# Kernel tuning notes

Measured on AMD Instinct MI355X. Metric: run time of the kernel, lower is better.

Reference implementation:

```python
import jax, jax.numpy as jnp
import numpy as np

B, T, C = 2, 2048, 1024
N_HEAD, N_GROUP = 16, 4
N_KV = N_HEAD // N_GROUP          # 4
HEAD_DIM = C // N_HEAD            # 64
ROPE_BASE = 10000.0
INIT_STD = 0.02


def setup_inputs() -> dict:
    key = jax.random.key(0)
    ks = jax.random.split(key, 5)
    kvC = N_KV * HEAD_DIM
    return {
        "x": jax.random.normal(ks[0], (B, T, C), jnp.float32),
        "w_q": jax.random.normal(ks[1], (C, C), jnp.float32) * INIT_STD,
        "b_q": jnp.zeros((C,), jnp.float32),
        "w_k": jax.random.normal(ks[2], (C, kvC), jnp.float32) * INIT_STD,
        "b_k": jnp.zeros((kvC,), jnp.float32),
        "w_v": jax.random.normal(ks[3], (C, kvC), jnp.float32) * INIT_STD,
        "b_v": jnp.zeros((kvC,), jnp.float32),
        "w_o": jax.random.normal(ks[4], (C, C), jnp.float32) * INIT_STD,
        "b_o": jnp.zeros((C,), jnp.float32),
    }


def reference(x, w_q, b_q, w_k, b_k, w_v, b_v, w_o, b_o):
    Bx, Tx, Cx = x.shape
    # projections (torch Linear math with weights stored as [in, out])
    q = (x @ w_q + b_q).reshape(Bx, Tx, N_HEAD, HEAD_DIM).transpose(0, 2, 1, 3)  # [B,H,T,hd]
    k = (x @ w_k + b_k).reshape(Bx, Tx, N_KV, HEAD_DIM).transpose(0, 2, 1, 3)    # [B,KV,T,hd]
    v = (x @ w_v + b_v).reshape(Bx, Tx, N_KV, HEAD_DIM).transpose(0, 2, 1, 3)

    # RoPE with INTERLEAVED pair convention: pairs are (dim 2i, dim 2i+1)
    inv_freq = 1.0 / (ROPE_BASE ** (jnp.arange(0, HEAD_DIM, 2, dtype=jnp.float32) / HEAD_DIM))
    freqs = jnp.arange(Tx, dtype=jnp.float32)[:, None] * inv_freq[None, :]       # [T, hd/2]
    cos, sin = jnp.cos(freqs), jnp.sin(freqs)

    def rope(t):
        tp = t.reshape(*t.shape[:-1], HEAD_DIM // 2, 2)
        e, o = tp[..., 0], tp[..., 1]          # even/odd lanes, [B,h,T,hd/2]
        er = e * cos - o * sin
        orr = e * sin + o * cos
        return jnp.stack([er, orr], axis=-1).reshape(t.shape)

    q, k = rope(q), rope(k)

    # GQA: duplicate each KV head n_group times (consecutively, like repeat_interleave)
    k = jnp.repeat(k, N_GROUP, axis=1)   # [B,H,T,hd]
    v = jnp.repeat(v, N_GROUP, axis=1)

    attn = jnp.einsum('bhqd,bhkd->bhqk', q, k) / np.sqrt(HEAD_DIM).astype(np.float32)
    causal = jnp.tril(jnp.ones((Tx, Tx), bool))
    attn = jnp.where(causal, attn, -jnp.inf)
    attn = jax.nn.softmax(attn, axis=-1)

    out = jnp.einsum('bhqk,bhkd->bhqd', attn, v)            # [B,H,T,hd]
    out = out.transpose(0, 2, 1, 3).reshape(Bx, Tx, Cx)
    return out @ w_o + b_o
```

## Files before the change

kernel.cpp:

```cpp
#include <hip/hip_runtime.h>
#include <hip/hip_bf16.h>

typedef __hip_bfloat16 bf16;
typedef __attribute__((ext_vector_type(8))) short short8_t;
typedef __attribute__((ext_vector_type(4))) short short4_t;
typedef __attribute__((ext_vector_type(4))) float f32x4;

#define B_SZ   2
#define T_SEQ  2048
#define C_DIM  1024
#define NH     16
#define NKV    4
#define HD     64
#define QKVW   1536

#define LOG2_BASE_OVER_32 0.4152410118609203f
#define Q_SCALE 0.1803368801111204f

__device__ __forceinline__ short f2bs(float f) {
    unsigned u = __float_as_uint(f);
    u += 0x7FFFu + ((u >> 16) & 1u);
    return (short)(u >> 16);
}
__device__ __forceinline__ short f2bs_trunc(float f) {
    return (short)(__float_as_uint(f) >> 16);
}
__device__ __forceinline__ float bs2f(short s) {
    unsigned u = ((unsigned)(unsigned short)s) << 16;
    return __uint_as_float(u);
}

__device__ __forceinline__ void store_c(float* p, float v) { *p = v; }
__device__ __forceinline__ void store_c(short* p, float v) { *p = f2bs(v); }

__device__ __forceinline__ void transpose_tile(
    const float* __restrict__ W, short* __restrict__ Wt,
    int K, int N, int n0, int k0, int tid)
{
    __shared__ float tile[32][33];
    int tx = tid & 31, ty = tid >> 5;
    #pragma unroll
    for (int i = 0; i < 4; ++i)
        tile[ty + 8 * i][tx] = W[(size_t)(k0 + ty + 8 * i) * N + n0 + tx];
    __syncthreads();
    #pragma unroll
    for (int i = 0; i < 4; ++i)
        Wt[(size_t)(n0 + ty + 8 * i) * K + k0 + tx] = f2bs(tile[tx][ty + 8 * i]);
}

__global__ __launch_bounds__(256) void prep_kernel(
    const float* __restrict__ x,
    const float* __restrict__ w_q, const float* __restrict__ w_k,
    const float* __restrict__ w_v, const float* __restrict__ w_o,
    const float* __restrict__ b_q, const float* __restrict__ b_k,
    const float* __restrict__ b_v,
    short* __restrict__ Xb, short* __restrict__ Wqkv, short* __restrict__ Wto,
    float* __restrict__ Bqkv, float2* __restrict__ Tab)
{
    int blk = blockIdx.x, tid = threadIdx.x;
    if (blk < 4096) {
        int i = blk * 1024 + tid * 4;
        float4 v = *(const float4*)(x + i);
        short4_t o;
        o[0] = f2bs(v.x); o[1] = f2bs(v.y); o[2] = f2bs(v.z); o[3] = f2bs(v.w);
        *(short4_t*)(Xb + i) = o;
    } else if (blk < 5120) {
        int l = blk - 4096;
        transpose_tile(w_q, Wqkv, C_DIM, C_DIM, (l & 31) * 32, (l >> 5) * 32, tid);
    } else if (blk < 5376) {
        int l = blk - 5120;
        transpose_tile(w_k, Wqkv + (size_t)1024 * C_DIM, C_DIM, 256,
                       (l & 7) * 32, (l >> 3) * 32, tid);
    } else if (blk < 5632) {
        int l = blk - 5376;
        transpose_tile(w_v, Wqkv + (size_t)1280 * C_DIM, C_DIM, 256,
                       (l & 7) * 32, (l >> 3) * 32, tid);
    } else if (blk < 6656) {
        int l = blk - 5632;
        transpose_tile(w_o, Wto, C_DIM, C_DIM, (l & 31) * 32, (l >> 5) * 32, tid);
    } else if (blk < 6662) {
        int i = (blk - 6656) * 256 + tid;
        float v;
        if (i < 1024)      v = b_q[i];
        else if (i < 1280) v = b_k[i - 1024];
        else               v = b_v[i - 1280];
        Bqkv[i] = v;
    } else {
        int idx = (blk - 6662) * 256 + tid;
        int t = idx >> 5, i = idx & 31;
        float ang = (float)t * exp2f(-(float)i * LOG2_BASE_OVER_32);
        Tab[idx] = make_float2(cosf(ang), sinf(ang));
    }
}

template <typename CT>
__global__ __launch_bounds__(256) void gemm_mfma_bt(
    const short* __restrict__ A, const short* __restrict__ Bt,
    const float* __restrict__ bias, CT* __restrict__ C,
    int M, int N, int K)
{
    __shared__ __align__(16) short sA[2][128][40];
    __shared__ __align__(16) short sB[2][128][40];

    int m0 = blockIdx.y * 128;
    int n0 = blockIdx.x * 128;
    int tid  = threadIdx.x;
    int w    = tid >> 6, lane = tid & 63;
    int quad = lane >> 4, l16 = lane & 15;
    int wm = w & 1, wn = w >> 1;

    f32x4 acc[4][4] = {};

    short8_t ra[2], rb[2];
    #pragma unroll
    for (int it = 0; it < 2; ++it) {
        int slot = tid + 256 * it, row = slot >> 2, g = (slot & 3) * 8;
        ra[it] = *(const short8_t*)(A  + (size_t)(m0 + row) * K + g);
        rb[it] = *(const short8_t*)(Bt + (size_t)(n0 + row) * K + g);
    }

    int buf = 0;
    for (int k0 = 0; k0 < K; k0 += 32, buf ^= 1) {
        #pragma unroll
        for (int it = 0; it < 2; ++it) {
            int slot = tid + 256 * it, row = slot >> 2, g = (slot & 3) * 8;
            *(short8_t*)&sA[buf][row][g] = ra[it];
            *(short8_t*)&sB[buf][row][g] = rb[it];
        }
        if (k0 + 32 < K) {
            #pragma unroll
            for (int it = 0; it < 2; ++it) {
                int slot = tid + 256 * it, row = slot >> 2, g = (slot & 3) * 8;
                ra[it] = *(const short8_t*)(A  + (size_t)(m0 + row) * K + k0 + 32 + g);
                rb[it] = *(const short8_t*)(Bt + (size_t)(n0 + row) * K + k0 + 32 + g);
            }
        }
        __syncthreads();

        short8_t af[4], bfr[4];
        #pragma unroll
        for (int mt = 0; mt < 4; ++mt)
            af[mt] = *(const short8_t*)&sA[buf][wm * 64 + mt * 16 + l16][quad * 8];
        #pragma unroll
        for (int nt = 0; nt < 4; ++nt)
            bfr[nt] = *(const short8_t*)&sB[buf][wn * 64 + nt * 16 + l16][quad * 8];
        #pragma unroll
        for (int mt = 0; mt < 4; ++mt)
            #pragma unroll
            for (int nt = 0; nt < 4; ++nt)
                acc[mt][nt] = __builtin_amdgcn_mfma_f32_16x16x32_bf16(
                    af[mt], bfr[nt], acc[mt][nt], 0, 0, 0);
    }

    #pragma unroll
    for (int mt = 0; mt < 4; ++mt) {
        #pragma unroll
        for (int nt = 0; nt < 4; ++nt) {
            int col = n0 + wn * 64 + nt * 16 + l16;
            float bv = bias[col];
            #pragma unroll
            for (int r = 0; r < 4; ++r) {
                int row = m0 + wm * 64 + mt * 16 + quad * 4 + r;
                store_c(&C[(size_t)row * N + col], acc[mt][nt][r] + bv);
            }
        }
    }
}

__global__ __launch_bounds__(256) void rope_k_transpose_v(
    short* __restrict__ QKV, const float2* __restrict__ Tab,
    short* __restrict__ Vt)
{
    int blk = blockIdx.x, tid = threadIdx.x;
    if (blk < 2048) {
        int g = blk * 256 + tid;
        int row = g >> 7, pi = g & 127;
        int col = 1024 + pi * 2;
        int t = row & (T_SEQ - 1);
        int i = pi & 31;
        size_t base = (size_t)row * QKVW + col;
        float e = bs2f(QKV[base]);
        float o = bs2f(QKV[base + 1]);
        float2 cs = Tab[t * 32 + i];
        QKV[base]     = f2bs(e * cs.x - o * cs.y);
        QKV[base + 1] = f2bs(e * cs.y + o * cs.x);
    } else {
        __shared__ __align__(16) short sT[64][72];
        int l = blk - 2048;
        int d0 = (l >> 6) * 64;
        int r0 = (l & 63) * 64;
        int i0 = tid >> 3, seg = (tid & 7) * 8;
        #pragma unroll
        for (int it = 0; it < 2; ++it) {
            int i = i0 + 32 * it;
            *(short8_t*)&sT[i][seg] =
                *(const short8_t*)(QKV + (size_t)(r0 + i) * QKVW + 1280 + d0 + seg);
        }
        __syncthreads();
        #pragma unroll
        for (int it = 0; it < 2; ++it) {
            int d = i0 + 32 * it;
            short8_t o;
            #pragma unroll
            for (int k = 0; k < 8; ++k) o[k] = sT[seg + k][d];
            *(short8_t*)(Vt + (size_t)(d0 + d) * (B_SZ * T_SEQ) + r0 + seg) = o;
        }
    }
}

__global__ __launch_bounds__(256) void attn_mfma6(
    const short* __restrict__ QKV, const short* __restrict__ Vt,
    const float2* __restrict__ Tab, short* __restrict__ O)
{
    __shared__ __align__(16) short sK [64][72];
    __shared__ __align__(16) short sVt[64][72];
    __shared__ __align__(16) short sP [4][16][72];

    const int tid  = threadIdx.x;
    const int w    = tid >> 6;
    const int lane = tid & 63;
    const int quad = lane >> 4;
    const int l16  = lane & 15;

    int blk = blockIdx.x;
    int grp = blk & 7;
    int tq  = 127 - (blk >> 3);
    int kvh = grp & 3;
    int b   = grp >> 2;
    int h   = kvh * 4 + w;
    int ct  = tq >> 2;

    const short* qptr = QKV + ((size_t)(b * T_SEQ + tq * 16 + l16)) * QKVW + h * HD;
    short8_t q0r = *(const short8_t*)(qptr + quad * 8);
    short8_t q1r = *(const short8_t*)(qptr + quad * 8 + 32);
    int tg = tq * 16 + l16;
    const float2* tb = Tab + tg * 32 + quad * 4;
    short8_t qf0, qf1;
    #pragma unroll
    for (int j = 0; j < 4; ++j) {
        float2 cs0 = tb[j];
        float e0 = bs2f(q0r[2 * j]), o0 = bs2f(q0r[2 * j + 1]);
        qf0[2 * j]     = f2bs((e0 * cs0.x - o0 * cs0.y) * Q_SCALE);
        qf0[2 * j + 1] = f2bs((e0 * cs0.y + o0 * cs0.x) * Q_SCALE);
        float2 cs1 = tb[j + 16];
        float e1 = bs2f(q1r[2 * j]), o1 = bs2f(q1r[2 * j + 1]);
        qf1[2 * j]     = f2bs((e1 * cs1.x - o1 * cs1.y) * Q_SCALE);
        qf1[2 * j + 1] = f2bs((e1 * cs1.y + o1 * cs1.x) * Q_SCALE);
    }

    const short* kbase  = QKV + (size_t)b * T_SEQ * QKVW + 1024 + kvh * HD;
    const short* vtbase = Vt + (size_t)(kvh * HD) * (B_SZ * T_SEQ) + b * T_SEQ;

    float m_l = -INFINITY, l_l = 0.f;
    f32x4 oacc[4];
    #pragma unroll
    for (int dt = 0; dt < 4; ++dt) oacc[dt] = (f32x4){0.f, 0.f, 0.f, 0.f};

    const int kkey = tid >> 3, kd = (tid & 7) * 8;
    const int vdim = tid >> 3, vseg = (tid & 7) * 8;

    short8_t kr[2], vr[2];
    #pragma unroll
    for (int it = 0; it < 2; ++it) {
        kr[it] = *(const short8_t*)(kbase + (size_t)(kkey + 32 * it) * QKVW + kd);
        vr[it] = *(const short8_t*)(vtbase + (size_t)(vdim + 32 * it) * (B_SZ * T_SEQ) + vseg);
    }

    for (int c = 0; c <= ct; ++c) {
        __syncthreads();
        #pragma unroll
        for (int it = 0; it < 2; ++it) {
            *(short8_t*)&sK [kkey + 32 * it][kd]   = kr[it];
            *(short8_t*)&sVt[vdim + 32 * it][vseg] = vr[it];
        }
        __syncthreads();
        if (c < ct) {
            int jn = (c + 1) * 64;
            #pragma unroll
            for (int it = 0; it < 2; ++it) {
                kr[it] = *(const short8_t*)(kbase + (size_t)(jn + kkey + 32 * it) * QKVW + kd);
                vr[it] = *(const short8_t*)(vtbase + (size_t)(vdim + 32 * it) * (B_SZ * T_SEQ) + jn + vseg);
            }
        }

        f32x4 sacc[4];
        #pragma unroll
        for (int kt = 0; kt < 4; ++kt) {
            f32x4 z = {0.f, 0.f, 0.f, 0.f};
            short8_t kf0 = *(const short8_t*)&sK[l16 + 16 * kt][quad * 8];
            short8_t kf1 = *(const short8_t*)&sK[l16 + 16 * kt][quad * 8 + 32];
            z = __builtin_amdgcn_mfma_f32_16x16x32_bf16(kf0, qf0, z, 0, 0, 0);
            z = __builtin_amdgcn_mfma_f32_16x16x32_bf16(kf1, qf1, z, 0, 0, 0);
            sacc[kt] = z;
        }

        if (c == ct) {
            int j0 = c * 64;
            #pragma unroll
            for (int kt = 0; kt < 4; ++kt)
                #pragma unroll
                for (int r = 0; r < 4; ++r)
                    if (j0 + 16 * kt + quad * 4 + r > tg) sacc[kt][r] = -INFINITY;
        }

        float vmax = sacc[0][0];
        #pragma unroll
        for (int kt = 0; kt < 4; ++kt)
            #pragma unroll
            for (int r = 0; r < 4; ++r) vmax = fmaxf(vmax, sacc[kt][r]);
        vmax = fmaxf(vmax, __shfl_xor(vmax, 16));
        vmax = fmaxf(vmax, __shfl_xor(vmax, 32));
        float mnew = fmaxf(m_l, vmax);
        float al = exp2f(m_l - mnew);
        m_l = mnew;

        float psum = 0.f;
        #pragma unroll
        for (int kt = 0; kt < 4; ++kt) {
            short4_t pk;
            #pragma unroll
            for (int r = 0; r < 4; ++r) {
                float p = exp2f(sacc[kt][r] - mnew);
                psum += p;
                pk[r] = f2bs_trunc(p);
            }
            *(short4_t*)&sP[w][l16][16 * kt + 4 * quad] = pk;
        }
        psum += __shfl_xor(psum, 16);
        psum += __shfl_xor(psum, 32);
        l_l = l_l * al + psum;

        if (__any(al < 1.f)) {
            #pragma unroll
            for (int r = 0; r < 4; ++r) {
                float alr = __shfl(al, quad * 4 + r);
                #pragma unroll
                for (int dt = 0; dt < 4; ++dt) oacc[dt][r] *= alr;
            }
        }

        short8_t pf0 = *(const short8_t*)&sP[w][l16][quad * 8];
        short8_t pf1 = *(const short8_t*)&sP[w][l16][quad * 8 + 32];
        #pragma unroll
        for (int dt = 0; dt < 4; ++dt) {
            short8_t vf0 = *(const short8_t*)&sVt[16 * dt + l16][quad * 8];
            short8_t vf1 = *(const short8_t*)&sVt[16 * dt + l16][quad * 8 + 32];
            oacc[dt] = __builtin_amdgcn_mfma_f32_16x16x32_bf16(pf0, vf0, oacc[dt], 0, 0, 0);
            oacc[dt] = __builtin_amdgcn_mfma_f32_16x16x32_bf16(pf1, vf1, oacc[dt], 0, 0, 0);
        }
    }

    #pragma unroll
    for (int r = 0; r < 4; ++r) {
        int m = quad * 4 + r;
        float lr = __shfl(l_l, quad * 4 + r);
        float inv = __builtin_amdgcn_rcpf(lr);
        #pragma unroll
        for (int dt = 0; dt < 4; ++dt)
            O[((size_t)b * T_SEQ + tq * 16 + m) * C_DIM + h * HD + 16 * dt + l16] =
                f2bs(oacc[dt][r] * inv);
    }
}

extern "C" void kernel_launch(void* const* d_in, const int* in_sizes, int n_in,
                              void* d_out, int out_size, void* d_ws, size_t ws_size,
                              hipStream_t stream)
{
    const float* x   = (const float*)d_in[0];
    const float* w_q = (const float*)d_in[1];
    const float* b_q = (const float*)d_in[2];
    const float* w_k = (const float*)d_in[3];
    const float* b_k = (const float*)d_in[4];
    const float* w_v = (const float*)d_in[5];
    const float* b_v = (const float*)d_in[6];
    const float* w_o = (const float*)d_in[7];
    const float* b_o = (const float*)d_in[8];
    float* out = (float*)d_out;

    char* ws = (char*)d_ws;
    short*  Xb   = (short*) (ws);
    short*  Ab   = (short*) (ws + ((size_t)8  << 20));
    short*  QKVb = (short*) (ws + ((size_t)16 << 20));
    short*  Wqkv = (short*) (ws + ((size_t)28 << 20));
    short*  Wto  = (short*) (ws + ((size_t)31 << 20));
    float*  Bqkv = (float*) (ws + ((size_t)33 << 20));
    float2* Tab  = (float2*)(ws + ((size_t)33 << 20) + 8192);
    short*  Vt   = (short*) (ws + ((size_t)34 << 20));

    const int M = B_SZ * T_SEQ;

    prep_kernel<<<6918, 256, 0, stream>>>(
        x, w_q, w_k, w_v, w_o, b_q, b_k, b_v, Xb, Wqkv, Wto, Bqkv, Tab);

    gemm_mfma_bt<short><<<dim3(QKVW / 128, M / 128), 256, 0, stream>>>(
        Xb, Wqkv, Bqkv, QKVb, M, QKVW, C_DIM);

    rope_k_transpose_v<<<2304, 256, 0, stream>>>(QKVb, Tab, Vt);

    attn_mfma6<<<B_SZ * NKV * 128, 256, 0, stream>>>(QKVb, Vt, Tab, Ab);

    gemm_mfma_bt<float><<<dim3(C_DIM / 128, M / 128), 256, 0, stream>>>(
        Ab, Wto, b_o, out, M, C_DIM, C_DIM);
}
```

Before: 181.5 us.

## Fuse RoPE, Q scaling and V transpose into QKV GEMM epilogue; widen attention key tiles

The QKV GEMM epilogue now applies RoPE and the softmax scale to Q and K columns, using a DPP lane swap to fetch the pair partner. For V column tiles it transposes the result through LDS and writes Vt directly. This removes the separate rope/transpose kernel and the per-block Q RoPE in attention. The attention kernel also processes 128-key chunks instead of 64, so causal loops take fewer iterations and barriers, in exchange for more LDS and registers and more masked work on the diagonal chunk.

```diff
diff --git a/kernel.cpp b/kernel.cpp
--- a/kernel.cpp
+++ b/kernel.cpp
@@ -13,6 +13,7 @@
 #define NKV    4
 #define HD     64
 #define QKVW   1536
+#define MTOK   (B_SZ * T_SEQ)
 
 #define LOG2_BASE_OVER_32 0.4152410118609203f
 #define Q_SCALE 0.1803368801111204f
@@ -29,9 +30,10 @@
     unsigned u = ((unsigned)(unsigned short)s) << 16;
     return __uint_as_float(u);
 }
-
-__device__ __forceinline__ void store_c(float* p, float v) { *p = v; }
-__device__ __forceinline__ void store_c(short* p, float v) { *p = f2bs(v); }
+__device__ __forceinline__ float dpp_xor1(float x) {
+    return __int_as_float(
+        __builtin_amdgcn_update_dpp(0, __float_as_int(x), 0xB1, 0xF, 0xF, true));
+}
 
 __device__ __forceinline__ void transpose_tile(
     const float* __restrict__ W, short* __restrict__ Wt,
@@ -93,15 +95,17 @@
     }
 }
 
-template <typename CT>
-__global__ __launch_bounds__(256) void gemm_mfma_bt(
+__global__ __launch_bounds__(256) void gemm_qkv(
     const short* __restrict__ A, const short* __restrict__ Bt,
-    const float* __restrict__ bias, CT* __restrict__ C,
-    int M, int N, int K)
-{
-    __shared__ __align__(16) short sA[2][128][40];
-    __shared__ __align__(16) short sB[2][128][40];
-
+    const float* __restrict__ bias, const float2* __restrict__ Tab,
+    short* __restrict__ QKVb, short* __restrict__ Vt)
+{
+    __shared__ __align__(16) short smem[20480];
+    typedef short lds_tile_t[128][40];
+    lds_tile_t* sA = (lds_tile_t*)smem;
+    lds_tile_t* sB = (lds_tile_t*)(smem + 10240);
+
+    const int K = C_DIM, N = QKVW;
     int m0 = blockIdx.y * 128;
     int n0 = blockIdx.x * 128;
     int tid  = threadIdx.x;
@@ -152,6 +156,111 @@
                     af[mt], bfr[nt], acc[mt][nt], 0, 0, 0);
     }
 
+    if (n0 < 1280) {
+        float scale = (n0 < 1024) ? Q_SCALE : 1.0f;
+        float sgn   = (l16 & 1) ? 1.0f : -1.0f;
+        #pragma unroll
+        for (int nt = 0; nt < 4; ++nt) {
+            int col = n0 + wn * 64 + nt * 16 + l16;
+            int ip  = (col & 63) >> 1;
+            float bv = bias[col];
+            #pragma unroll
+            for (int mt = 0; mt < 4; ++mt) {
+                #pragma unroll
+                for (int r = 0; r < 4; ++r) {
+                    int row = m0 + wm * 64 + mt * 16 + quad * 4 + r;
+                    float v = acc[mt][nt][r] + bv;
+                    float po = dpp_xor1(v);
+                    float2 cs = Tab[(row & (T_SEQ - 1)) * 32 + ip];
+                    float res = (v * cs.x + sgn * po * cs.y) * scale;
+                    QKVb[(size_t)row * QKVW + col] = f2bs(res);
+                }
+            }
+        }
+    } else {
+        __syncthreads();
+        short (*sT)[136] = (short(*)[136])smem;
+        #pragma unroll
+        for (int nt = 0; nt < 4; ++nt) {
+            int col_l = wn * 64 + nt * 16 + l16;
+            float bv = bias[n0 + col_l];
+            #pragma unroll
+            for (int mt = 0; mt < 4; ++mt)
+                #pragma unroll
+                for (int r = 0; r < 4; ++r)
+                    sT[col_l][wm * 64 + mt * 16 + quad * 4 + r] =
+                        f2bs(acc[mt][nt][r] + bv);
+        }
+        __syncthreads();
+        int d0 = n0 - 1280;
+        #pragma unroll
+        for (int it = 0; it < 8; ++it) {
+            int slot = tid + 256 * it;
+            int dl = slot >> 4, seg = (slot & 15) * 8;
+            *(short8_t*)(Vt + (size_t)(d0 + dl) * MTOK + m0 + seg) =
+                *(const short8_t*)&sT[dl][seg];
+        }
+    }
+}
+
+__global__ __launch_bounds__(256) void gemm_mfma_o(
+    const short* __restrict__ A, const short* __restrict__ Bt,
+    const float* __restrict__ bias, float* __restrict__ C,
+    int M, int N, int K)
+{
+    __shared__ __align__(16) short sA[2][128][40];
+    __shared__ __align__(16) short sB[2][128][40];
+
+    int m0 = blockIdx.y * 128;
+    int n0 = blockIdx.x * 128;
+    int tid  = threadIdx.x;
+    int w    = tid >> 6, lane = tid & 63;
+    int quad = lane >> 4, l16 = lane & 15;
+    int wm = w & 1, wn = w >> 1;
+
+    f32x4 acc[4][4] = {};
+
+    short8_t ra[2], rb[2];
+    #pragma unroll
+    for (int it = 0; it < 2; ++it) {
+        int slot = tid + 256 * it, row = slot >> 2, g = (slot & 3) * 8;
+        ra[it] = *(const short8_t*)(A  + (size_t)(m0 + row) * K + g);
+        rb[it] = *(const short8_t*)(Bt + (size_t)(n0 + row) * K + g);
+    }
+
+    int buf = 0;
+    for (int k0 = 0; k0 < K; k0 += 32, buf ^= 1) {
+        #pragma unroll
+        for (int it = 0; it < 2; ++it) {
+            int slot = tid + 256 * it, row = slot >> 2, g = (slot & 3) * 8;
+            *(short8_t*)&sA[buf][row][g] = ra[it];
+            *(short8_t*)&sB[buf][row][g] = rb[it];
+        }
+        if (k0 + 32 < K) {
+            #pragma unroll
+            for (int it = 0; it < 2; ++it) {
+                int slot = tid + 256 * it, row = slot >> 2, g = (slot & 3) * 8;
+                ra[it] = *(const short8_t*)(A  + (size_t)(m0 + row) * K + k0 + 32 + g);
+                rb[it] = *(const short8_t*)(Bt + (size_t)(n0 + row) * K + k0 + 32 + g);
+            }
+        }
+        __syncthreads();
+
+        short8_t af[4], bfr[4];
+        #pragma unroll
+        for (int mt = 0; mt < 4; ++mt)
+            af[mt] = *(const short8_t*)&sA[buf][wm * 64 + mt * 16 + l16][quad * 8];
+        #pragma unroll
+        for (int nt = 0; nt < 4; ++nt)
+            bfr[nt] = *(const short8_t*)&sB[buf][wn * 64 + nt * 16 + l16][quad * 8];
+        #pragma unroll
+        for (int mt = 0; mt < 4; ++mt)
+            #pragma unroll
+            for (int nt = 0; nt < 4; ++nt)
+                acc[mt][nt] = __builtin_amdgcn_mfma_f32_16x16x32_bf16(
+                    af[mt], bfr[nt], acc[mt][nt], 0, 0, 0);
+    }
+
     #pragma unroll
     for (int mt = 0; mt < 4; ++mt) {
         #pragma unroll
@@ -161,60 +270,19 @@
             #pragma unroll
             for (int r = 0; r < 4; ++r) {
                 int row = m0 + wm * 64 + mt * 16 + quad * 4 + r;
-                store_c(&C[(size_t)row * N + col], acc[mt][nt][r] + bv);
-            }
-        }
-    }
-}
-
-__global__ __launch_bounds__(256) void rope_k_transpose_v(
-    short* __restrict__ QKV, const float2* __restrict__ Tab,
-    short* __restrict__ Vt)
-{
-    int blk = blockIdx.x, tid = threadIdx.x;
-    if (blk < 2048) {
-        int g = blk * 256 + tid;
-        int row = g >> 7, pi = g & 127;
-        int col = 1024 + pi * 2;
-        int t = row & (T_SEQ - 1);
-        int i = pi & 31;
-        size_t base = (size_t)row * QKVW + col;
-        float e = bs2f(QKV[base]);
-        float o = bs2f(QKV[base + 1]);
-        float2 cs = Tab[t * 32 + i];
-        QKV[base]     = f2bs(e * cs.x - o * cs.y);
-        QKV[base + 1] = f2bs(e * cs.y + o * cs.x);
-    } else {
-        __shared__ __align__(16) short sT[64][72];
-        int l = blk - 2048;
-        int d0 = (l >> 6) * 64;
-        int r0 = (l & 63) * 64;
-        int i0 = tid >> 3, seg = (tid & 7) * 8;
-        #pragma unroll
-        for (int it = 0; it < 2; ++it) {
-            int i = i0 + 32 * it;
-            *(short8_t*)&sT[i][seg] =
-                *(const short8_t*)(QKV + (size_t)(r0 + i) * QKVW + 1280 + d0 + seg);
-        }
-        __syncthreads();
-        #pragma unroll
-        for (int it = 0; it < 2; ++it) {
-            int d = i0 + 32 * it;
-            short8_t o;
-            #pragma unroll
-            for (int k = 0; k < 8; ++k) o[k] = sT[seg + k][d];
-            *(short8_t*)(Vt + (size_t)(d0 + d) * (B_SZ * T_SEQ) + r0 + seg) = o;
-        }
-    }
-}
-
-__global__ __launch_bounds__(256) void attn_mfma6(
+                C[(size_t)row * N + col] = acc[mt][nt][r] + bv;
+            }
+        }
+    }
+}
+
+__global__ __launch_bounds__(256) void attn_mfma7(
     const short* __restrict__ QKV, const short* __restrict__ Vt,
-    const float2* __restrict__ Tab, short* __restrict__ O)
-{
-    __shared__ __align__(16) short sK [64][72];
-    __shared__ __align__(16) short sVt[64][72];
-    __shared__ __align__(16) short sP [4][16][72];
+    short* __restrict__ O)
+{
+    __shared__ __align__(16) short sK [128][72];
+    __shared__ __align__(16) short sVt[64][136];
+    __shared__ __align__(16) short sP [4][16][136];
 
     const int tid  = threadIdx.x;
     const int w    = tid >> 6;
@@ -228,64 +296,51 @@
     int kvh = grp & 3;
     int b   = grp >> 2;
     int h   = kvh * 4 + w;
-    int ct  = tq >> 2;
+    int ct  = (tq * 16 + 15) >> 7;
+    int tg  = tq * 16 + l16;
 
     const short* qptr = QKV + ((size_t)(b * T_SEQ + tq * 16 + l16)) * QKVW + h * HD;
-    short8_t q0r = *(const short8_t*)(qptr + quad * 8);
-    short8_t q1r = *(const short8_t*)(qptr + quad * 8 + 32);
-    int tg = tq * 16 + l16;
-    const float2* tb = Tab + tg * 32 + quad * 4;
-    short8_t qf0, qf1;
-    #pragma unroll
-    for (int j = 0; j < 4; ++j) {
-        float2 cs0 = tb[j];
-        float e0 = bs2f(q0r[2 * j]), o0 = bs2f(q0r[2 * j + 1]);
-        qf0[2 * j]     = f2bs((e0 * cs0.x - o0 * cs0.y) * Q_SCALE);
-        qf0[2 * j + 1] = f2bs((e0 * cs0.y + o0 * cs0.x) * Q_SCALE);
-        float2 cs1 = tb[j + 16];
-        float e1 = bs2f(q1r[2 * j]), o1 = bs2f(q1r[2 * j + 1]);
-        qf1[2 * j]     = f2bs((e1 * cs1.x - o1 * cs1.y) * Q_SCALE);
-        qf1[2 * j + 1] = f2bs((e1 * cs1.y + o1 * cs1.x) * Q_SCALE);
-    }
+    short8_t qf0 = *(const short8_t*)(qptr + quad * 8);
+    short8_t qf1 = *(const short8_t*)(qptr + quad * 8 + 32);
 
     const short* kbase  = QKV + (size_t)b * T_SEQ * QKVW + 1024 + kvh * HD;
-    const short* vtbase = Vt + (size_t)(kvh * HD) * (B_SZ * T_SEQ) + b * T_SEQ;
+    const short* vtbase = Vt + (size_t)(kvh * HD) * MTOK + b * T_SEQ;
 
     float m_l = -INFINITY, l_l = 0.f;
     f32x4 oacc[4];
     #pragma unroll
     for (int dt = 0; dt < 4; ++dt) oacc[dt] = (f32x4){0.f, 0.f, 0.f, 0.f};
 
-    const int kkey = tid >> 3, kd = (tid & 7) * 8;
-    const int vdim = tid >> 3, vseg = (tid & 7) * 8;
-
-    short8_t kr[2], vr[2];
-    #pragma unroll
-    for (int it = 0; it < 2; ++it) {
-        kr[it] = *(const short8_t*)(kbase + (size_t)(kkey + 32 * it) * QKVW + kd);
-        vr[it] = *(const short8_t*)(vtbase + (size_t)(vdim + 32 * it) * (B_SZ * T_SEQ) + vseg);
+    short8_t kr[4], vr[4];
+    #pragma unroll
+    for (int it = 0; it < 4; ++it) {
+        int slot = tid + 256 * it;
+        kr[it] = *(const short8_t*)(kbase + (size_t)(slot >> 3) * QKVW + (slot & 7) * 8);
+        vr[it] = *(const short8_t*)(vtbase + (size_t)(slot >> 4) * MTOK + (slot & 15) * 8);
     }
 
     for (int c = 0; c <= ct; ++c) {
         __syncthreads();
         #pragma unroll
-        for (int it = 0; it < 2; ++it) {
-            *(short8_t*)&sK [kkey + 32 * it][kd]   = kr[it];
-            *(short8_t*)&sVt[vdim + 32 * it][vseg] = vr[it];
+        for (int it = 0; it < 4; ++it) {
+            int slot = tid + 256 * it;
+            *(short8_t*)&sK [slot >> 3][(slot & 7) * 8]  = kr[it];
+            *(short8_t*)&sVt[slot >> 4][(slot & 15) * 8] = vr[it];
         }
         __syncthreads();
         if (c < ct) {
-            int jn = (c + 1) * 64;
-            #pragma unroll
-            for (int it = 0; it < 2; ++it) {
-                kr[it] = *(const short8_t*)(kbase + (size_t)(jn + kkey + 32 * it) * QKVW + kd);
-                vr[it] = *(const short8_t*)(vtbase + (size_t)(vdim + 32 * it) * (B_SZ * T_SEQ) + jn + vseg);
-            }
-        }
-
-        f32x4 sacc[4];
-        #pragma unroll
-        for (int kt = 0; kt < 4; ++kt) {
+            int jn = (c + 1) * 128;
+            #pragma unroll
+            for (int it = 0; it < 4; ++it) {
+                int slot = tid + 256 * it;
+                kr[it] = *(const short8_t*)(kbase + (size_t)(jn + (slot >> 3)) * QKVW + (slot & 7) * 8);
+                vr[it] = *(const short8_t*)(vtbase + (size_t)(slot >> 4) * MTOK + jn + (slot & 15) * 8);
+            }
+        }
+
+        f32x4 sacc[8];
+        #pragma unroll
+        for (int kt = 0; kt < 8; ++kt) {
             f32x4 z = {0.f, 0.f, 0.f, 0.f};
             short8_t kf0 = *(const short8_t*)&sK[l16 + 16 * kt][quad * 8];
             short8_t kf1 = *(const short8_t*)&sK[l16 + 16 * kt][quad * 8 + 32];
@@ -295,9 +350,9 @@
         }
 
         if (c == ct) {
-            int j0 = c * 64;
-            #pragma unroll
-            for (int kt = 0; kt < 4; ++kt)
+            int j0 = c * 128;
+            #pragma unroll
+            for (int kt = 0; kt < 8; ++kt)
                 #pragma unroll
                 for (int r = 0; r < 4; ++r)
                     if (j0 + 16 * kt + quad * 4 + r > tg) sacc[kt][r] = -INFINITY;
@@ -305,7 +360,7 @@
 
         float vmax = sacc[0][0];
         #pragma unroll
-        for (int kt = 0; kt < 4; ++kt)
+        for (int kt = 0; kt < 8; ++kt)
             #pragma unroll
             for (int r = 0; r < 4; ++r) vmax = fmaxf(vmax, sacc[kt][r]);
         vmax = fmaxf(vmax, __shfl_xor(vmax, 16));
@@ -316,7 +371,7 @@
 
         float psum = 0.f;
         #pragma unroll
-        for (int kt = 0; kt < 4; ++kt) {
+        for (int kt = 0; kt < 8; ++kt) {
             short4_t pk;
             #pragma unroll
             for (int r = 0; r < 4; ++r) {
@@ -339,14 +394,17 @@
             }
         }
 
-        short8_t pf0 = *(const short8_t*)&sP[w][l16][quad * 8];
-        short8_t pf1 = *(const short8_t*)&sP[w][l16][quad * 8 + 32];
+        short8_t pf[4];
+        #pragma unroll
+        for (int g = 0; g < 4; ++g)
+            pf[g] = *(const short8_t*)&sP[w][l16][32 * g + quad * 8];
         #pragma unroll
         for (int dt = 0; dt < 4; ++dt) {
-            short8_t vf0 = *(const short8_t*)&sVt[16 * dt + l16][quad * 8];
-            short8_t vf1 = *(const short8_t*)&sVt[16 * dt + l16][quad * 8 + 32];
-            oacc[dt] = __builtin_amdgcn_mfma_f32_16x16x32_bf16(pf0, vf0, oacc[dt], 0, 0, 0);
-            oacc[dt] = __builtin_amdgcn_mfma_f32_16x16x32_bf16(pf1, vf1, oacc[dt], 0, 0, 0);
+            #pragma unroll
+            for (int g = 0; g < 4; ++g) {
+                short8_t vf = *(const short8_t*)&sVt[16 * dt + l16][32 * g + quad * 8];
+                oacc[dt] = __builtin_amdgcn_mfma_f32_16x16x32_bf16(pf[g], vf, oacc[dt], 0, 0, 0);
+            }
         }
     }
 
@@ -387,18 +445,16 @@
     float2* Tab  = (float2*)(ws + ((size_t)33 << 20) + 8192);
     short*  Vt   = (short*) (ws + ((size_t)34 << 20));
 
-    const int M = B_SZ * T_SEQ;
+    const int M = MTOK;
 
     prep_kernel<<<6918, 256, 0, stream>>>(
         x, w_q, w_k, w_v, w_o, b_q, b_k, b_v, Xb, Wqkv, Wto, Bqkv, Tab);
 
-    gemm_mfma_bt<short><<<dim3(QKVW / 128, M / 128), 256, 0, stream>>>(
-        Xb, Wqkv, Bqkv, QKVb, M, QKVW, C_DIM);
-
-    rope_k_transpose_v<<<2304, 256, 0, stream>>>(QKVb, Tab, Vt);
-
-    attn_mfma6<<<B_SZ * NKV * 128, 256, 0, stream>>>(QKVb, Vt, Tab, Ab);
-
-    gemm_mfma_bt<float><<<dim3(C_DIM / 128, M / 128), 256, 0, stream>>>(
+    gemm_qkv<<<dim3(QKVW / 128, M / 128), 256, 0, stream>>>(
+        Xb, Wqkv, Bqkv, Tab, QKVb, Vt);
+
+    attn_mfma7<<<B_SZ * NKV * 128, 256, 0, stream>>>(QKVb, Vt, Ab);
+
+    gemm_mfma_o<<<dim3(C_DIM / 128, M / 128), 256, 0, stream>>>(
         Ab, Wto, b_o, out, M, C_DIM, C_DIM);
 }
```

After: 183.9 us. Within noise of the previous version (+1.3%).
